# Optimization experiments

Measured on AMD Instinct MI355X. Metric: run time of the kernel, lower is better.

The kernel has to match this reference:

```python
import jax, jax.numpy as jnp
import numpy as np

N_NODES = 50000
N_EDGES = 1600000
HIDDEN = 512
LN_EPS = 1e-5


def setup_inputs() -> dict:
    key = jax.random.key(0)
    k1, k2, k3, k4 = jax.random.split(key, 4)
    label_emb = jax.random.normal(k1, (N_NODES, HIDDEN), dtype=jnp.float32)
    edge_index = jax.random.randint(k2, (2, N_EDGES), 0, N_NODES, dtype=jnp.int64)
    W = jax.random.normal(k3, (HIDDEN, HIDDEN), dtype=jnp.float32) / np.sqrt(HIDDEN)
    b = jnp.zeros((HIDDEN,), dtype=jnp.float32)
    gamma = jnp.ones((HIDDEN,), dtype=jnp.float32)
    beta = jnp.zeros((HIDDEN,), dtype=jnp.float32)
    return {"label_emb": label_emb, "edge_index": edge_index, "W": W, "b": b,
            "gamma": gamma, "beta": beta}


def _gcn_conv(x, src, dst, W, b, n_nodes):
    loops = jnp.arange(n_nodes, dtype=src.dtype)
    src_all = jnp.concatenate([src, loops])  # [E+N]
    dst_all = jnp.concatenate([dst, loops])
    ones = jnp.ones_like(dst_all, dtype=x.dtype)
    deg = jax.ops.segment_sum(ones, dst_all, num_segments=n_nodes)  # [N]
    dinv = jnp.where(deg > 0, jax.lax.rsqrt(deg), 0.0)
    norm = dinv[src_all] * dinv[dst_all]  # [E+N]
    h = x @ W  # [N, H] dense transform first (fewer FLOPs than per-edge)
    msgs = h[src_all] * norm[:, None]  # gather + per-edge scale
    out = jax.ops.segment_sum(msgs, dst_all, num_segments=n_nodes)  # scatter-add
    return out + b


def reference(label_emb, edge_index, W, b, gamma, beta):
    residual = label_emb
    src, dst = edge_index[0], edge_index[1]
    h = _gcn_conv(label_emb, src, dst, W, b, N_NODES)
    # dropout is identity at inference (training=False)
    h = residual + h
    mean = jnp.mean(h, axis=-1, keepdims=True)
    var = jnp.var(h, axis=-1, keepdims=True)
    h = (h - mean) * jax.lax.rsqrt(var + LN_EPS) * gamma + beta
    return h
```

## Files before the change

### kernel.cpp

```cpp
#include <hip/hip_runtime.h>
#include <hip/hip_bf16.h>

#define HID 512
#define CAP 128
#define BINCAP 384

typedef unsigned int uint32;
using bf16x8 = __attribute__((ext_vector_type(8))) short;
using f32x4  = __attribute__((ext_vector_type(4))) float;
using f32x2  = __attribute__((ext_vector_type(2))) float;
using u32x2  = __attribute__((ext_vector_type(2))) unsigned int;
using u32x4  = __attribute__((ext_vector_type(4))) unsigned int;
using u16x4  = __attribute__((ext_vector_type(4))) unsigned short;
using u16x8  = __attribute__((ext_vector_type(8))) unsigned short;

__device__ __forceinline__ unsigned short f2bf(float f) {
    uint32 u = __float_as_uint(f);
    uint32 r = (u + 0x7FFFu + ((u >> 16) & 1u)) >> 16;
    return (unsigned short)r;
}

__device__ __forceinline__ void gl_lds16(const void* g, void* l) {
    __builtin_amdgcn_global_load_lds(
        (const __attribute__((address_space(1))) void*)g,
        (__attribute__((address_space(3))) void*)l,
        16, 0, 0);
}

__device__ __forceinline__ bf16x8 pack_bf16x8(f32x4 lo, f32x4 hi) {
    union { bf16x8 v; unsigned short u[8]; } r;
    #pragma unroll
    for (int z = 0; z < 4; ++z) {
        union { __hip_bfloat16 h; unsigned short u; } a, b;
        a.h = __float2bfloat16(lo[z]);
        b.h = __float2bfloat16(hi[z]);
        r.u[z] = a.u; r.u[z + 4] = b.u;
    }
    return r.v;
}

__global__ __launch_bounds__(256) void prep_bin(const int* __restrict__ src,
                                                const int* __restrict__ dst,
                                                int* __restrict__ bincnt,
                                                uint32* __restrict__ bins, int e,
                                                const float* __restrict__ W,
                                                unsigned short* __restrict__ Wt,
                                                int nbb) {
    const int bid = blockIdx.x;
    if (bid < nbb) {
        for (int i = bid * 256 + (int)threadIdx.x; i < e; i += nbb * 256) {
            int d = dst[i], s = src[i];
            int b = d >> 3;
            int p = atomicAdd(&bincnt[b], 1);
            bins[(size_t)b * BINCAP + p] = ((uint32)(d & 7) << 16) | (uint32)s;
        }
    } else {
        int idx = (bid - nbb) * 256 + threadIdx.x;
        if (idx < HID * HID) {
            int k = idx >> 9, n = idx & (HID - 1);
            Wt[n * HID + k] = f2bf(W[k * HID + n]);
        }
    }
}

#define NWGX 4
__global__ __launch_bounds__(256) void csr_gemm(const uint32* __restrict__ bins,
                                                const int* __restrict__ bincnt,
                                                unsigned short* __restrict__ csrf,
                                                int* __restrict__ fill,
                                                float* __restrict__ dinvf,
                                                const float* __restrict__ Xf,
                                                const unsigned short* __restrict__ Wt,
                                                unsigned char* __restrict__ hs8,
                                                int nslices, int nwg, int nreal) {
    __shared__ alignas(16) unsigned char smem[49152];

    if ((int)blockIdx.x < nslices) {
        unsigned short* lcs = (unsigned short*)smem;
        int* lcnt = (int*)(smem + 128 * CAP * 2);
        const int b = blockIdx.x;
        for (int j = threadIdx.x; j < 128; j += 256) lcnt[j] = 0;
        __syncthreads();
        #pragma unroll
        for (int sb = 0; sb < 16; ++sb) {
            const int gb = b * 16 + sb;
            const int m = bincnt[gb];
            const uint32* be = bins + (size_t)gb * BINCAP;
            for (int i = threadIdx.x; i < m; i += 256) {
                uint32 ev = be[i];
                int ln = sb * 8 + (int)(ev >> 16);
                int p = atomicAdd(&lcnt[ln], 1);
                lcs[ln * CAP + p] = (unsigned short)(ev & 0xFFFFu);
            }
        }
        __syncthreads();
        u32x4* gout = (u32x4*)(csrf + (size_t)b * 128 * CAP);
        const u32x4* lin = (const u32x4*)lcs;
        for (int j = threadIdx.x; j < 128 * CAP / 8; j += 256) gout[j] = lin[j];
        if (threadIdx.x < 128) {
            int c = lcnt[threadIdx.x];
            fill[b * 128 + threadIdx.x] = c;
            dinvf[b * 128 + threadIdx.x] = rsqrtf((float)c + 1.0f);
        }
        return;
    }

    float* Aldsf = (float*)smem;
    unsigned short* Blds = (unsigned short*)(smem + 32768);
    const int bx = (int)blockIdx.x - nslices;
    const int cpx = nwg >> 3;
    const int swz = (bx & 7) * cpx + (bx >> 3);
    const int row_base = (swz >> 2) * 128;
    const int col_base = (swz & 3) * 128;

    const int t = threadIdx.x;
    const int lane = t & 63, wid = t >> 6;
    const int wm = wid >> 1, wn = wid & 1;

    const int arow4 = lane >> 4;
    const int ach   = (lane & 15) >> 1;
    const int ahalf = lane & 1;
    const int srow = lane >> 3;
    const int gch  = ((lane & 7) ^ srow) * 8;
    const unsigned short* gB = Wt + (size_t)(col_base + wid * 8 + srow) * HID + gch;
    unsigned short* lB = &Blds[wid * 512];

    f32x4 acc[4][4];
    #pragma unroll
    for (int m = 0; m < 4; ++m)
        #pragma unroll
        for (int n = 0; n < 4; ++n)
            acc[m][n] = (f32x4){0.f, 0.f, 0.f, 0.f};

    const int rr = lane & 15;
    const int kg8 = lane >> 4;

    for (int k0 = 0; k0 < HID; k0 += 64) {
        #pragma unroll
        for (int rd = 0; rd < 8; ++rd) {
            int r = wid * 32 + rd * 4 + arow4;
            int grow = row_base + r;
            if (grow >= nreal) grow = nreal - 1;
            int sw = ((ach ^ (r & 7)) << 3) + ahalf * 4;
            gl_lds16(Xf + (size_t)grow * HID + k0 + sw,
                     Aldsf + (size_t)(wid * 32 + rd * 4) * 64);
        }
        #pragma unroll
        for (int rd = 0; rd < 4; ++rd)
            gl_lds16(gB + (size_t)rd * 32 * HID + k0, lB + rd * 2048);
        __syncthreads();

        bf16x8 afr[4][2], bfr[4][2];
        #pragma unroll
        for (int m = 0; m < 4; ++m) {
            int row = wm * 64 + m * 16 + rr;
            #pragma unroll
            for (int ks = 0; ks < 2; ++ks) {
                int off = (((ks * 4 + kg8) ^ (row & 7)) << 3);
                const float* ap = &Aldsf[(size_t)(row << 6) + off];
                f32x4 lo = *(const f32x4*)ap;
                f32x4 hi = *(const f32x4*)(ap + 4);
                afr[m][ks] = pack_bf16x8(lo, hi);
            }
        }
        #pragma unroll
        for (int n = 0; n < 4; ++n) {
            int row = wn * 64 + n * 16 + rr;
            #pragma unroll
            for (int ks = 0; ks < 2; ++ks)
                bfr[n][ks] = *(const bf16x8*)&Blds[row * 64 + (((ks * 4 + kg8) ^ (row & 7)) * 8)];
        }
        #pragma unroll
        for (int ks = 0; ks < 2; ++ks)
            #pragma unroll
            for (int m = 0; m < 4; ++m)
                #pragma unroll
                for (int n = 0; n < 4; ++n)
                    acc[m][n] = __builtin_amdgcn_mfma_f32_16x16x32_bf16(afr[m][ks], bfr[n][ks], acc[m][n], 0, 0, 0);
        __syncthreads();
    }

    const int rgrp = (lane >> 4) * 4;
    const int cc = lane & 15;
    #pragma unroll
    for (int m = 0; m < 4; ++m) {
        #pragma unroll
        for (int r = 0; r < 4; ++r) {
            int grow = row_base + wm * 64 + m * 16 + rgrp + r;
            #pragma unroll
            for (int n = 0; n < 4; ++n) {
                int gcol = col_base + wn * 64 + n * 16 + cc;
                float v = acc[m][n][r];
                unsigned int p = __builtin_amdgcn_cvt_pk_fp8_f32(v, v, 0u, false);
                hs8[(size_t)grow * HID + gcol] = (unsigned char)p;
            }
        }
    }
}

__device__ __forceinline__ void dec8s(u32x2 v, float g, float* acc) {
    f32x2 a = __builtin_amdgcn_cvt_pk_f32_fp8(v[0], false);
    f32x2 b = __builtin_amdgcn_cvt_pk_f32_fp8(v[0], true);
    f32x2 c = __builtin_amdgcn_cvt_pk_f32_fp8(v[1], false);
    f32x2 d = __builtin_amdgcn_cvt_pk_f32_fp8(v[1], true);
    acc[0] += g * a[0]; acc[1] += g * a[1]; acc[2] += g * b[0]; acc[3] += g * b[1];
    acc[4] += g * c[0]; acc[5] += g * c[1]; acc[6] += g * d[0]; acc[7] += g * d[1];
}

__global__ __launch_bounds__(256) void agg_ln(const unsigned char* __restrict__ hs8,
                                              const float* __restrict__ resid,
                                              const float* __restrict__ bvec,
                                              const float* __restrict__ gamma,
                                              const float* __restrict__ beta,
                                              const int* __restrict__ fill,
                                              const float* __restrict__ dinvf,
                                              const unsigned short* __restrict__ csrf,
                                              float* __restrict__ out, int nn) {
    const int wave = threadIdx.x >> 6;
    const int lane = threadIdx.x & 63;
    const int n = blockIdx.x * 4 + wave;
    if (n >= nn) return;
    const int c0 = lane * 8;

    const float gn = dinvf[n];
    float acc[8];
    #pragma unroll
    for (int j = 0; j < 8; ++j) acc[j] = 0.f;
    dec8s(*(const u32x2*)(hs8 + (size_t)n * HID + c0), gn, acc);

    const int m = fill[n];
    const unsigned short* idx = csrf + (size_t)n * CAP;
    int i = 0;
    for (; i + 8 <= m; i += 8) {
        u16x8 iv = *(const u16x8*)(idx + i);
        float g0 = dinvf[iv[0]], g1 = dinvf[iv[1]], g2 = dinvf[iv[2]], g3 = dinvf[iv[3]];
        float g4 = dinvf[iv[4]], g5 = dinvf[iv[5]], g6 = dinvf[iv[6]], g7 = dinvf[iv[7]];
        u32x2 v0 = *(const u32x2*)(hs8 + (size_t)iv[0] * HID + c0);
        u32x2 v1 = *(const u32x2*)(hs8 + (size_t)iv[1] * HID + c0);
        u32x2 v2 = *(const u32x2*)(hs8 + (size_t)iv[2] * HID + c0);
        u32x2 v3 = *(const u32x2*)(hs8 + (size_t)iv[3] * HID + c0);
        u32x2 v4 = *(const u32x2*)(hs8 + (size_t)iv[4] * HID + c0);
        u32x2 v5 = *(const u32x2*)(hs8 + (size_t)iv[5] * HID + c0);
        u32x2 v6 = *(const u32x2*)(hs8 + (size_t)iv[6] * HID + c0);
        u32x2 v7 = *(const u32x2*)(hs8 + (size_t)iv[7] * HID + c0);
        dec8s(v0, g0, acc); dec8s(v1, g1, acc); dec8s(v2, g2, acc); dec8s(v3, g3, acc);
        dec8s(v4, g4, acc); dec8s(v5, g5, acc); dec8s(v6, g6, acc); dec8s(v7, g7, acc);
    }
    for (; i < m; ++i) {
        int s = idx[i];
        dec8s(*(const u32x2*)(hs8 + (size_t)s * HID + c0), dinvf[s], acc);
    }

    f32x4 r0 = __builtin_nontemporal_load((const f32x4*)(resid + (size_t)n * HID + c0));
    f32x4 r1 = __builtin_nontemporal_load((const f32x4*)(resid + (size_t)n * HID + c0 + 4));
    float val[8];
    #pragma unroll
    for (int j = 0; j < 4; ++j) {
        val[j]     = r0[j] + gn * acc[j]     + bvec[c0 + j];
        val[j + 4] = r1[j] + gn * acc[j + 4] + bvec[c0 + j + 4];
    }

    float s = 0.f, q = 0.f;
    #pragma unroll
    for (int j = 0; j < 8; ++j) { s += val[j]; q += val[j] * val[j]; }
    #pragma unroll
    for (int off = 32; off > 0; off >>= 1) {
        s += __shfl_xor(s, off, 64);
        q += __shfl_xor(q, off, 64);
    }
    const float mean = s * (1.f / 512.f);
    const float var = q * (1.f / 512.f) - mean * mean;
    const float rstd = rsqrtf(var + 1e-5f);

    f32x4 o0, o1;
    #pragma unroll
    for (int j = 0; j < 4; ++j) {
        o0[j] = (val[j]     - mean) * rstd * gamma[c0 + j]     + beta[c0 + j];
        o1[j] = (val[j + 4] - mean) * rstd * gamma[c0 + j + 4] + beta[c0 + j + 4];
    }
    __builtin_nontemporal_store(o0, (f32x4*)(out + (size_t)n * HID + c0));
    __builtin_nontemporal_store(o1, (f32x4*)(out + (size_t)n * HID + c0 + 4));
}

extern "C" void kernel_launch(void* const* d_in, const int* in_sizes, int n_in,
                              void* d_out, int out_size, void* d_ws, size_t ws_size,
                              hipStream_t stream) {
    const float* X     = (const float*)d_in[0];
    const int*   edges = (const int*)d_in[1];
    const float* W     = (const float*)d_in[2];
    const float* b     = (const float*)d_in[3];
    const float* gamma = (const float*)d_in[4];
    const float* beta  = (const float*)d_in[5];
    float* out = (float*)d_out;

    const int E = in_sizes[1] / 2;
    const int N = in_sizes[0] / HID;
    const int M_pad = ((N + 255) / 256) * 256;
    const int nslices = M_pad / 128;
    const int nbins = M_pad / 8;
    const int* src = edges;
    const int* dst = edges + E;

    char* w = (char*)d_ws;
    auto alloc = [&](size_t bytes) { char* p = w; w += (bytes + 255) & ~(size_t)255; return p; };
    int*    fill   = (int*)alloc((size_t)M_pad * 4);
    float*  dinvf  = (float*)alloc((size_t)M_pad * 4);
    int*    bincnt = (int*)alloc((size_t)nbins * 4);
    uint32* bins   = (uint32*)alloc((size_t)nbins * BINCAP * 4);
    unsigned short* csrf = (unsigned short*)alloc((size_t)M_pad * CAP * 2);
    unsigned short* Wt   = (unsigned short*)alloc((size_t)HID * HID * 2);
    unsigned char*  hs8  = (unsigned char*)alloc((size_t)M_pad * HID);

    hipMemsetAsync(bincnt, 0, (size_t)nbins * 4, stream);

    const int nbb = 2048;
    const int nbw = (HID * HID + 255) / 256;
    prep_bin<<<nbb + nbw, 256, 0, stream>>>(src, dst, bincnt, bins, E, W, Wt, nbb);

    const int nwg = (M_pad / 128) * NWGX;
    csr_gemm<<<nslices + nwg, 256, 0, stream>>>(bins, bincnt, csrf, fill, dinvf,
                                                X, Wt, hs8, nslices, nwg, N);

    agg_ln<<<(N + 3) / 4, 256, 0, stream>>>(hs8, X, b, gamma, beta, fill, dinvf, csrf, out, N);
}
```

Measured before the change: 272.3 us.

## Overlap edge binning with GEMM and split bin-to-CSR into its own kernel

Edge binning moves out of the first kernel and into the GEMM launch, interleaved as one binning block per eight GEMM blocks, so the atomic-heavy scatter runs alongside the matrix multiply. The memset of bin counters is folded into the weight-transpose kernel, and the bin-to-CSR pass becomes a separate kernel that runs after both. The goal is to hide the binning latency behind GEMM compute and drop a memset launch. In exchange there is one extra kernel launch, and the GEMM blocks now compete with 196 binning blocks for CU slots.

```diff
diff --git a/kernel.cpp b/kernel.cpp
--- a/kernel.cpp
+++ b/kernel.cpp
@@ -11,7 +11,6 @@
 using f32x2  = __attribute__((ext_vector_type(2))) float;
 using u32x2  = __attribute__((ext_vector_type(2))) unsigned int;
 using u32x4  = __attribute__((ext_vector_type(4))) unsigned int;
-using u16x4  = __attribute__((ext_vector_type(4))) unsigned short;
 using u16x8  = __attribute__((ext_vector_type(8))) unsigned short;
 
 __device__ __forceinline__ unsigned short f2bf(float f) {
@@ -39,77 +38,53 @@
     return r.v;
 }
 
-__global__ __launch_bounds__(256) void prep_bin(const int* __restrict__ src,
+__global__ __launch_bounds__(256) void wt_prep(const float* __restrict__ W,
+                                               unsigned short* __restrict__ Wt,
+                                               int* __restrict__ bincnt, int nbins,
+                                               int nbw) {
+    const int bid = blockIdx.x;
+    if (bid < nbw) {
+        int idx = bid * 256 + threadIdx.x;
+        if (idx < HID * HID) {
+            int k = idx >> 9, n = idx & (HID - 1);
+            Wt[n * HID + k] = f2bf(W[k * HID + n]);
+        }
+    } else {
+        int i = (bid - nbw) * 256 + threadIdx.x;
+        if (i < nbins) bincnt[i] = 0;
+    }
+}
+
+#define NWGX 4
+#define NBINB 196
+__global__ __launch_bounds__(256) void gemm_bin(const int* __restrict__ src,
                                                 const int* __restrict__ dst,
                                                 int* __restrict__ bincnt,
                                                 uint32* __restrict__ bins, int e,
-                                                const float* __restrict__ W,
-                                                unsigned short* __restrict__ Wt,
-                                                int nbb) {
-    const int bid = blockIdx.x;
-    if (bid < nbb) {
-        for (int i = bid * 256 + (int)threadIdx.x; i < e; i += nbb * 256) {
+                                                const float* __restrict__ Xf,
+                                                const unsigned short* __restrict__ Wt,
+                                                unsigned char* __restrict__ hs8,
+                                                int nwg, int nreal) {
+    __shared__ alignas(16) unsigned char smem[49152];
+
+    const int grp = (int)blockIdx.x / 9;
+    const int l9  = (int)blockIdx.x % 9;
+    if (l9 == 8) {
+        const int stride = NBINB * 256;
+        for (int i = grp * 256 + (int)threadIdx.x; i < e; i += stride) {
             int d = dst[i], s = src[i];
             int b = d >> 3;
             int p = atomicAdd(&bincnt[b], 1);
             bins[(size_t)b * BINCAP + p] = ((uint32)(d & 7) << 16) | (uint32)s;
         }
-    } else {
-        int idx = (bid - nbb) * 256 + threadIdx.x;
-        if (idx < HID * HID) {
-            int k = idx >> 9, n = idx & (HID - 1);
-            Wt[n * HID + k] = f2bf(W[k * HID + n]);
-        }
-    }
-}
-
-#define NWGX 4
-__global__ __launch_bounds__(256) void csr_gemm(const uint32* __restrict__ bins,
-                                                const int* __restrict__ bincnt,
-                                                unsigned short* __restrict__ csrf,
-                                                int* __restrict__ fill,
-                                                float* __restrict__ dinvf,
-                                                const float* __restrict__ Xf,
-                                                const unsigned short* __restrict__ Wt,
-                                                unsigned char* __restrict__ hs8,
-                                                int nslices, int nwg, int nreal) {
-    __shared__ alignas(16) unsigned char smem[49152];
-
-    if ((int)blockIdx.x < nslices) {
-        unsigned short* lcs = (unsigned short*)smem;
-        int* lcnt = (int*)(smem + 128 * CAP * 2);
-        const int b = blockIdx.x;
-        for (int j = threadIdx.x; j < 128; j += 256) lcnt[j] = 0;
-        __syncthreads();
-        #pragma unroll
-        for (int sb = 0; sb < 16; ++sb) {
-            const int gb = b * 16 + sb;
-            const int m = bincnt[gb];
-            const uint32* be = bins + (size_t)gb * BINCAP;
-            for (int i = threadIdx.x; i < m; i += 256) {
-                uint32 ev = be[i];
-                int ln = sb * 8 + (int)(ev >> 16);
-                int p = atomicAdd(&lcnt[ln], 1);
-                lcs[ln * CAP + p] = (unsigned short)(ev & 0xFFFFu);
-            }
-        }
-        __syncthreads();
-        u32x4* gout = (u32x4*)(csrf + (size_t)b * 128 * CAP);
-        const u32x4* lin = (const u32x4*)lcs;
-        for (int j = threadIdx.x; j < 128 * CAP / 8; j += 256) gout[j] = lin[j];
-        if (threadIdx.x < 128) {
-            int c = lcnt[threadIdx.x];
-            fill[b * 128 + threadIdx.x] = c;
-            dinvf[b * 128 + threadIdx.x] = rsqrtf((float)c + 1.0f);
-        }
         return;
     }
 
+    const int ord = grp * 8 + l9;
     float* Aldsf = (float*)smem;
     unsigned short* Blds = (unsigned short*)(smem + 32768);
-    const int bx = (int)blockIdx.x - nslices;
     const int cpx = nwg >> 3;
-    const int swz = (bx & 7) * cpx + (bx >> 3);
+    const int swz = (ord & 7) * cpx + (ord >> 3);
     const int row_base = (swz >> 2) * 128;
     const int col_base = (swz & 3) * 128;
 
@@ -195,6 +170,39 @@
                 hs8[(size_t)grow * HID + gcol] = (unsigned char)p;
             }
         }
+    }
+}
+
+__global__ __launch_bounds__(256) void bin2csr(const uint32* __restrict__ bins,
+                                               const int* __restrict__ bincnt,
+                                               unsigned short* __restrict__ csrf,
+                                               int* __restrict__ fill,
+                                               float* __restrict__ dinvf) {
+    __shared__ alignas(16) unsigned short lcs[128 * CAP];
+    __shared__ int lcnt[128];
+    const int b = blockIdx.x;
+    for (int j = threadIdx.x; j < 128; j += 256) lcnt[j] = 0;
+    __syncthreads();
+    #pragma unroll
+    for (int sb = 0; sb < 16; ++sb) {
+        const int gb = b * 16 + sb;
+        const int m = bincnt[gb];
+        const uint32* be = bins + (size_t)gb * BINCAP;
+        for (int i = threadIdx.x; i < m; i += 256) {
+            uint32 ev = be[i];
+            int ln = sb * 8 + (int)(ev >> 16);
+            int p = atomicAdd(&lcnt[ln], 1);
+            lcs[ln * CAP + p] = (unsigned short)(ev & 0xFFFFu);
+        }
+    }
+    __syncthreads();
+    u32x4* gout = (u32x4*)(csrf + (size_t)b * 128 * CAP);
+    const u32x4* lin = (const u32x4*)lcs;
+    for (int j = threadIdx.x; j < 128 * CAP / 8; j += 256) gout[j] = lin[j];
+    if (threadIdx.x < 128) {
+        int c = lcnt[threadIdx.x];
+        fill[b * 128 + threadIdx.x] = c;
+        dinvf[b * 128 + threadIdx.x] = rsqrtf((float)c + 1.0f);
     }
 }
 
@@ -311,15 +319,15 @@
     unsigned short* Wt   = (unsigned short*)alloc((size_t)HID * HID * 2);
     unsigned char*  hs8  = (unsigned char*)alloc((size_t)M_pad * HID);
 
-    hipMemsetAsync(bincnt, 0, (size_t)nbins * 4, stream);
-
-    const int nbb = 2048;
     const int nbw = (HID * HID + 255) / 256;
-    prep_bin<<<nbb + nbw, 256, 0, stream>>>(src, dst, bincnt, bins, E, W, Wt, nbb);
+    const int nbz = (nbins + 255) / 256;
+    wt_prep<<<nbw + nbz, 256, 0, stream>>>(W, Wt, bincnt, nbins, nbw);
 
     const int nwg = (M_pad / 128) * NWGX;
-    csr_gemm<<<nslices + nwg, 256, 0, stream>>>(bins, bincnt, csrf, fill, dinvf,
-                                                X, Wt, hs8, nslices, nwg, N);
+    gemm_bin<<<(nwg / 8) * 9, 256, 0, stream>>>(src, dst, bincnt, bins, E,
+                                                X, Wt, hs8, nwg, N);
+
+    bin2csr<<<nslices, 256, 0, stream>>>(bins, bincnt, csrf, fill, dinvf);
 
     agg_ln<<<(N + 3) / 4, 256, 0, stream>>>(hs8, X, b, gamma, beta, fill, dinvf, csrf, out, N);
 }
```

Result: slower. 283.7 us (+4.2%).
